# Performance work log

Hardware: AMD Instinct MI355X
Metric: run time of the kernel (lower is better)

Reference implementation:

```python
import jax, jax.numpy as jnp
import numpy as np

N = 1 << 20   # number of values to quantize
K = 256       # codebook size (8-bit)


def setup_inputs() -> dict:
    key = jax.random.key(0)
    kx, kc = jax.random.split(key)
    x = jax.random.normal(kx, (N,), dtype=jnp.float32)
    centers = jax.random.normal(kc, (K,), dtype=jnp.float32)
    return {"x": x, "centers": centers}


def reference(x, centers):
    # (x[:, None] - centers[None, :]).abs().argmin(dim=1)
    # -> index of nearest scalar codebook entry per element, shape (N,)
    diff = jnp.abs(x[:, None] - centers[None, :])  # (N, K)
    return jnp.argmin(diff, axis=1)
```

## Files before the change

kernel.cpp:

```cpp
#include <hip/hip_runtime.h>
#include <cfloat>

#define N_ELEM (1 << 20)
#define K_CENTERS 256
#define EPT 8
#define BLOCK 256

__global__ __launch_bounds__(BLOCK) void kmeans_argmin_brute(
    const float* __restrict__ x,
    const float* __restrict__ centers,
    int* __restrict__ out)
{
    const int base = (blockIdx.x * BLOCK + threadIdx.x) * EPT;

    float4 a = *reinterpret_cast<const float4*>(x + base);
    float4 b = *reinterpret_cast<const float4*>(x + base + 4);
    float xs[EPT] = {a.x, a.y, a.z, a.w, b.x, b.y, b.z, b.w};

    float bd[EPT];
    int   bi[EPT];
#pragma unroll
    for (int e = 0; e < EPT; ++e) { bd[e] = FLT_MAX; bi[e] = 0; }

#pragma unroll 16
    for (int k = 0; k < K_CENTERS; ++k) {
        const float c = centers[k];
#pragma unroll
        for (int e = 0; e < EPT; ++e) {
            float d = fabsf(xs[e] - c);
            if (d < bd[e]) { bd[e] = d; bi[e] = k; }
        }
    }

    *reinterpret_cast<int4*>(out + base)     = make_int4(bi[0], bi[1], bi[2], bi[3]);
    *reinterpret_cast<int4*>(out + base + 4) = make_int4(bi[4], bi[5], bi[6], bi[7]);
}

extern "C" void kernel_launch(void* const* d_in, const int* in_sizes, int n_in,
                              void* d_out, int out_size, void* d_ws, size_t ws_size,
                              hipStream_t stream)
{
    const float* x       = (const float*)d_in[0];
    const float* centers = (const float*)d_in[1];
    int*         out     = (int*)d_out;

    const int grid = N_ELEM / (BLOCK * EPT);
    kmeans_argmin_brute<<<grid, BLOCK, 0, stream>>>(x, centers, out);
}
```

Measured before the change: 83.43 us.

## Replace brute-force nearest-center scan with sorted codebook and binary search

Adds a one-block kernel that sorts the 256 centers by rank counting into workspace, keeping their original indices. The main kernel loads the sorted codebook into shared memory and finds each element's nearest center with a branchless binary search plus a two-neighbour comparison. Ties pick the lower original index. This cuts the per-element work from 256 compare steps to about 9 shared-memory lookups, at the cost of a second kernel launch and dependent LDS accesses.

```diff
diff --git a/kernel.cpp b/kernel.cpp
--- a/kernel.cpp
+++ b/kernel.cpp
@@ -1,39 +1,69 @@
 #include <hip/hip_runtime.h>
-#include <cfloat>
 
 #define N_ELEM (1 << 20)
-#define K_CENTERS 256
-#define EPT 8
+#define K 256
 #define BLOCK 256
+#define EPT 4
+#define GRID (N_ELEM / (BLOCK * EPT))
 
-__global__ __launch_bounds__(BLOCK) void kmeans_argmin_brute(
+
+__global__ __launch_bounds__(K) void sort_centers_kernel(
+    const float* __restrict__ centers,
+    float* __restrict__ ws_val,
+    int*   __restrict__ ws_idx)
+{
+    __shared__ float sc[K];
+    const int t = threadIdx.x;
+    const float c = centers[t];
+    sc[t] = c;
+    __syncthreads();
+
+    int rank = 0;
+#pragma unroll 8
+    for (int j = 0; j < K; ++j) {
+        float cj = sc[j];
+        rank += (cj < c) || (cj == c && j < t);
+    }
+    ws_val[rank] = c;
+    ws_idx[rank] = t;
+}
+
+__global__ __launch_bounds__(BLOCK) void argmin_bsearch_kernel(
     const float* __restrict__ x,
-    const float* __restrict__ centers,
-    int* __restrict__ out)
+    const float* __restrict__ ws_val,
+    const int*   __restrict__ ws_idx,
+    int*         __restrict__ out)
 {
-    const int base = (blockIdx.x * BLOCK + threadIdx.x) * EPT;
+    __shared__ float s_val[K];
+    __shared__ int   s_idx[K];
+    const int t = threadIdx.x;
+    s_val[t] = ws_val[t];
+    s_idx[t] = ws_idx[t];
+    __syncthreads();
 
-    float4 a = *reinterpret_cast<const float4*>(x + base);
-    float4 b = *reinterpret_cast<const float4*>(x + base + 4);
-    float xs[EPT] = {a.x, a.y, a.z, a.w, b.x, b.y, b.z, b.w};
+    const int base = (blockIdx.x * BLOCK + t) * EPT;
+    float4 v = *reinterpret_cast<const float4*>(x + base);
+    float xs[EPT] = {v.x, v.y, v.z, v.w};
+    int res[EPT];
 
-    float bd[EPT];
-    int   bi[EPT];
 #pragma unroll
-    for (int e = 0; e < EPT; ++e) { bd[e] = FLT_MAX; bi[e] = 0; }
+    for (int e = 0; e < EPT; ++e) {
+        const float xv = xs[e];
+        int pos = 0;
+#pragma unroll
+        for (int s = 128; s > 0; s >>= 1)
+            pos += (s_val[pos + s - 1] < xv) ? s : 0;
+        pos += (s_val[pos] < xv) ? 1 : 0;
 
-#pragma unroll 16
-    for (int k = 0; k < K_CENTERS; ++k) {
-        const float c = centers[k];
-#pragma unroll
-        for (int e = 0; e < EPT; ++e) {
-            float d = fabsf(xs[e] - c);
-            if (d < bd[e]) { bd[e] = d; bi[e] = k; }
-        }
+        const int il = (pos > 0)  ? pos - 1 : 0;
+        const int ir = (pos < K)  ? pos     : K - 1;
+        const float dl = fabsf(xv - s_val[il]);
+        const float dr = fabsf(xv - s_val[ir]);
+        const int ol = s_idx[il], orr = s_idx[ir];
+        res[e] = (dl < dr) ? ol : ((dr < dl) ? orr : min(ol, orr));
     }
 
-    *reinterpret_cast<int4*>(out + base)     = make_int4(bi[0], bi[1], bi[2], bi[3]);
-    *reinterpret_cast<int4*>(out + base + 4) = make_int4(bi[4], bi[5], bi[6], bi[7]);
+    *reinterpret_cast<int4*>(out + base) = make_int4(res[0], res[1], res[2], res[3]);
 }
 
 extern "C" void kernel_launch(void* const* d_in, const int* in_sizes, int n_in,
@@ -44,6 +74,9 @@
     const float* centers = (const float*)d_in[1];
     int*         out     = (int*)d_out;
 
-    const int grid = N_ELEM / (BLOCK * EPT);
-    kmeans_argmin_brute<<<grid, BLOCK, 0, stream>>>(x, centers, out);
+    float* ws_val = (float*)d_ws;
+    int*   ws_idx = (int*)(ws_val + K);
+
+    sort_centers_kernel<<<1, K, 0, stream>>>(centers, ws_val, ws_idx);
+    argmin_bsearch_kernel<<<GRID, BLOCK, 0, stream>>>(x, ws_val, ws_idx, out);
 }
```

New measurement: 67.62 us. -18.9%, faster.
